# Kernel tuning notes

Measured on AMD Instinct MI355X. Metric: run time of the kernel, lower is better.

## Reference

```python
import jax, jax.numpy as jnp
import numpy as np

V, P, C, L, H = 50257, 1024, 768, 12, 12  # vocab, block_size, n_embd, n_layer, n_head
HD = C // H                                # head_dim = 64
B, T = 2, 1024
STD = 0.02
EPS = 1e-5


def setup_inputs() -> dict:
    key = jax.random.key(0)
    ks = jax.random.split(key, 8)
    n = lambda k, shape: (jax.random.normal(k, shape, dtype=jnp.float32) * STD)
    return dict(
        idx=jax.random.randint(ks[0], (B, T), 0, V),
        wte=n(ks[1], (V, C)),
        wpe=n(ks[2], (P, C)),
        ln1_g=jnp.ones((L, C), jnp.float32), ln1_b=jnp.zeros((L, C), jnp.float32),
        attn_w=n(ks[3], (L, C, 3 * C)), attn_b=jnp.zeros((L, 3 * C), jnp.float32),
        proj_w=n(ks[4], (L, C, C)), proj_b=jnp.zeros((L, C), jnp.float32),
        ln2_g=jnp.ones((L, C), jnp.float32), ln2_b=jnp.zeros((L, C), jnp.float32),
        fc_w=n(ks[5], (L, C, 4 * C)), fc_b=jnp.zeros((L, 4 * C), jnp.float32),
        fp_w=n(ks[6], (L, 4 * C, C)), fp_b=jnp.zeros((L, C), jnp.float32),
        lnf_g=jnp.ones((C,), jnp.float32), lnf_b=jnp.zeros((C,), jnp.float32),
    )


def _ln(x, g, b):
    m = jnp.mean(x, axis=-1, keepdims=True)
    v = jnp.var(x, axis=-1, keepdims=True)
    return (x - m) * jax.lax.rsqrt(v + EPS) * g + b


def _block(x, p):
    (g1, b1, aw, ab, pw, pb, g2, b2, fw, fb, fpw, fpb) = p
    Bd, Td, Cd = x.shape
    # attention
    h = _ln(x, g1, b1)
    qkv = h @ aw + ab                                  # [B,T,3C]
    qkv = qkv.reshape(Bd, Td, H, 3 * HD)               # faithful to reshape(B,T,H,3*hd)
    q, k, v = jnp.split(qkv, 3, axis=-1)               # each [B,T,H,hd]
    scale = jnp.asarray(1.0 / np.sqrt(HD), x.dtype)
    att = jnp.einsum('bthd,bshd->bhts', q, k) * scale  # [B,H,T,T]
    mask = jnp.tril(jnp.ones((Td, Td), x.dtype))
    att = att * mask - 1e9 * (1.0 - mask)
    att = jax.nn.softmax(att, axis=-1)
    o = jnp.einsum('bhts,bshd->bthd', att, v).reshape(Bd, Td, Cd)
    x = x + (o @ pw + pb)
    # MLP (exact gelu, as TF keras 'gelu' default)
    h2 = _ln(x, g2, b2)
    x = x + (jax.nn.gelu(h2 @ fw + fb, approximate=False) @ fpw + fpb)
    return x


def reference(idx, wte, wpe, ln1_g, ln1_b, attn_w, attn_b, proj_w, proj_b,
              ln2_g, ln2_b, fc_w, fc_b, fp_w, fp_b, lnf_g, lnf_b):
    Td = idx.shape[1]
    x = wte[idx] + wpe[:Td]                            # [B,T,C]
    layers = (ln1_g, ln1_b, attn_w, attn_b, proj_w, proj_b,
              ln2_g, ln2_b, fc_w, fc_b, fp_w, fp_b)

    def step(carry, p):
        return _block(carry, p), None

    x, _ = jax.lax.scan(step, x, layers)
    x = _ln(x, lnf_g, lnf_b)
    logits = x @ wte.T                                 # tied embedding head [B,T,V]
    return logits
```

## Files before the change

kernel.cpp:

```cpp
#include <hip/hip_runtime.h>
#include <cstdint>
#include <cstddef>

#define BT   2048
#define TT   1024
#define CC   768
#define HH   12
#define LL   12
#define VV   50257
#define VPAD 50304

typedef __attribute__((ext_vector_type(8))) short short8;
typedef __attribute__((ext_vector_type(4))) float float4v;

__device__ __forceinline__ short f2bf(float f) {
  union { float f; uint32_t u; } v; v.f = f;
  uint32_t r = v.u + 0x7FFFu + ((v.u >> 16) & 1u);
  return (short)(r >> 16);
}

__device__ __forceinline__ void gl2lds16(const short* g, const short* lds_base) {
  __builtin_amdgcn_global_load_lds(
      (const __attribute__((address_space(1))) void*)g,
      (__attribute__((address_space(3))) void*)lds_base, 16, 0, 0);
}

__global__ __launch_bounds__(256) void cast_pad_kernel(const float* __restrict__ in,
                                                       short* __restrict__ out,
                                                       long n_in, long n_out) {
  long i = ((long)blockIdx.x * 256 + threadIdx.x) * 4;
  if (i >= n_out) return;
#pragma unroll
  for (int j = 0; j < 4; ++j) {
    long k = i + j;
    if (k < n_out) out[k] = (k < n_in) ? f2bf(in[k]) : (short)0;
  }
}

__global__ __launch_bounds__(256) void transpose_cast_kernel(const float* __restrict__ in,
                                                             short* __restrict__ out,
                                                             int K, int N) {
  __shared__ float tile[32][33];
  int n0 = blockIdx.x * 32, k0 = blockIdx.y * 32;
  int c = threadIdx.x & 31, r = threadIdx.x >> 5;
#pragma unroll
  for (int rr = 0; rr < 32; rr += 8)
    tile[rr + r][c] = in[(size_t)(k0 + rr + r) * N + n0 + c];
  __syncthreads();
#pragma unroll
  for (int rr = 0; rr < 32; rr += 8)
    out[(size_t)(n0 + rr + r) * K + k0 + c] = f2bf(tile[c][rr + r]);
}

__global__ __launch_bounds__(256) void embed_kernel(const int* __restrict__ idx,
                                                    const float* __restrict__ wte,
                                                    const float* __restrict__ wpe,
                                                    float* __restrict__ x) {
  int row = blockIdx.x, tid = threadIdx.x;
  int tok = idx[row];
  int t = row & (TT - 1);
#pragma unroll
  for (int kk = 0; kk < 3; ++kk) {
    int c = tid + kk * 256;
    x[(size_t)row * CC + c] = wte[(size_t)tok * CC + c] + wpe[(size_t)t * CC + c];
  }
}

__global__ __launch_bounds__(256) void ln_kernel(const float* __restrict__ x,
                                                 const float* __restrict__ g,
                                                 const float* __restrict__ bta,
                                                 short* __restrict__ out) {
  int row = blockIdx.x, tid = threadIdx.x;
  const float* xr = x + (size_t)row * CC;
  float v0 = xr[tid], v1 = xr[tid + 256], v2 = xr[tid + 512];
  float s = v0 + v1 + v2;
#pragma unroll
  for (int off = 32; off >= 1; off >>= 1) s += __shfl_xor(s, off, 64);
  __shared__ float red[8];
  int wid = tid >> 6;
  if ((tid & 63) == 0) red[wid] = s;
  __syncthreads();
  float mean = (red[0] + red[1] + red[2] + red[3]) * (1.0f / CC);
  float d0 = v0 - mean, d1 = v1 - mean, d2 = v2 - mean;
  float q = d0 * d0 + d1 * d1 + d2 * d2;
#pragma unroll
  for (int off = 32; off >= 1; off >>= 1) q += __shfl_xor(q, off, 64);
  if ((tid & 63) == 0) red[4 + wid] = q;
  __syncthreads();
  float var = (red[4] + red[5] + red[6] + red[7]) * (1.0f / CC);
  float rstd = rsqrtf(var + 1e-5f);
  out[(size_t)row * CC + tid]       = f2bf(d0 * rstd * g[tid]       + bta[tid]);
  out[(size_t)row * CC + tid + 256] = f2bf(d1 * rstd * g[tid + 256] + bta[tid + 256]);
  out[(size_t)row * CC + tid + 512] = f2bf(d2 * rstd * g[tid + 512] + bta[tid + 512]);
}

template <int MODE>
__global__ __launch_bounds__(256) void gemm_nt(const short* __restrict__ A,
                                               const short* __restrict__ Bt,
                                               const float* __restrict__ bias,
                                               float* __restrict__ resf,
                                               short* __restrict__ outb,
                                               float* __restrict__ outf,
                                               int K, int ldo, int Nvalid) {
  __shared__ __align__(16) short As[128 * 32];
  __shared__ __align__(16) short Bs[128 * 32];
  const int tid = threadIdx.x;
  const int w = tid >> 6, lane = tid & 63, quad = lane >> 4, l16 = lane & 15;
  const int wr = w & 1, wc = w >> 1;
  const int m0 = blockIdx.y * 128, n0 = blockIdx.x * 128;

  float4v acc[4][4];
#pragma unroll
  for (int i = 0; i < 4; ++i)
#pragma unroll
    for (int j = 0; j < 4; ++j) acc[i][j] = float4v{0.f, 0.f, 0.f, 0.f};

  const int r0 = tid >> 2;
  const int c0 = (tid & 3) * 8;
  const short* ga0 = A  + (size_t)(m0 + r0) * K + c0;
  const short* ga1 = A  + (size_t)(m0 + 64 + r0) * K + c0;
  const short* gb0 = Bt + (size_t)(n0 + r0) * K + c0;
  const short* gb1 = Bt + (size_t)(n0 + 64 + r0) * K + c0;
  const short* lA0 = As + w * 512;
  const short* lA1 = As + 2048 + w * 512;
  const short* lB0 = Bs + w * 512;
  const short* lB1 = Bs + 2048 + w * 512;

  const int kTiles = K >> 5;
  for (int kt = 0; kt < kTiles; ++kt) {
    const int ko = kt * 32;
    __syncthreads();
    gl2lds16(ga0 + ko, lA0);
    gl2lds16(ga1 + ko, lA1);
    gl2lds16(gb0 + ko, lB0);
    gl2lds16(gb1 + ko, lB1);
    __syncthreads();
    short8 af[4], bfr[4];
#pragma unroll
    for (int t = 0; t < 4; ++t) {
      af[t]  = *(const short8*)&As[(wr * 64 + t * 16 + l16) * 32 + quad * 8];
      bfr[t] = *(const short8*)&Bs[(wc * 64 + t * 16 + l16) * 32 + quad * 8];
    }
#pragma unroll
    for (int i = 0; i < 4; ++i)
#pragma unroll
      for (int j = 0; j < 4; ++j)
        acc[i][j] = __builtin_amdgcn_mfma_f32_16x16x32_bf16(af[i], bfr[j], acc[i][j], 0, 0, 0);
  }

#pragma unroll
  for (int i = 0; i < 4; ++i) {
#pragma unroll
    for (int j = 0; j < 4; ++j) {
#pragma unroll
      for (int r = 0; r < 4; ++r) {
        int gm = m0 + wr * 64 + i * 16 + quad * 4 + r;
        int gn = n0 + wc * 64 + j * 16 + l16;
        float v = acc[i][j][r];
        if (MODE == 0) {
          outb[(size_t)gm * ldo + gn] = f2bf(v + bias[gn]);
        } else if (MODE == 1) {
          size_t o = (size_t)gm * ldo + gn;
          resf[o] = resf[o] + v + bias[gn];
        } else if (MODE == 2) {
          float t = v + bias[gn];
          float gl = 0.5f * t * (1.0f + erff(t * 0.70710678118654752f));
          outb[(size_t)gm * ldo + gn] = f2bf(gl);
        } else {
          if (gn < Nvalid) outf[(size_t)gm * ldo + gn] = v;
        }
      }
    }
  }
}

__global__ __launch_bounds__(256) void attn_kernel(const short* __restrict__ qkv,
                                                   short* __restrict__ o) {
  __shared__ __align__(16) short Vt[64 * 32];
  __shared__ __align__(16) short Pl[4][16 * 32];
  const int tid = threadIdx.x;
  const int w = tid >> 6, lane = tid & 63, quad = lane >> 4, l16 = lane & 15;
  const int b = blockIdx.z, h = blockIdx.y, q0 = blockIdx.x * 64;
  const size_t rs = 3 * CC;
  const size_t base = (size_t)b * TT * rs + (size_t)h * 192;

  short8 qa[2];
  {
    int t = q0 + w * 16 + l16;
    const short* qp = qkv + base + (size_t)t * rs + quad * 8;
    qa[0] = *(const short8*)(qp);
    qa[1] = *(const short8*)(qp + 32);
  }
  float4v oacc[4];
#pragma unroll
  for (int i = 0; i < 4; ++i) oacc[i] = float4v{0.f, 0.f, 0.f, 0.f};
  float mrun[4] = {-1e30f, -1e30f, -1e30f, -1e30f};
  float lrun[4] = {0.f, 0.f, 0.f, 0.f};

  const int nst = q0 / 32 + 2;
  for (int st = 0; st < nst; ++st) {
    const int s0 = st * 32;
    __syncthreads();
    {
      int sl = tid >> 3;
      int d0 = (tid & 7) * 8;
      const short* vp = qkv + base + (size_t)(s0 + sl) * rs + 128 + d0;
      short8 v8 = *(const short8*)vp;
#pragma unroll
      for (int j = 0; j < 8; ++j) Vt[(d0 + j) * 32 + sl] = v8[j];
    }
    __syncthreads();

    float4v S[2];
#pragma unroll
    for (int nt = 0; nt < 2; ++nt) {
      int s = s0 + nt * 16 + l16;
      const short* kp = qkv + base + (size_t)s * rs + 64 + quad * 8;
      short8 kb0 = *(const short8*)kp;
      short8 kb1 = *(const short8*)(kp + 32);
      float4v z = float4v{0.f, 0.f, 0.f, 0.f};
      z = __builtin_amdgcn_mfma_f32_16x16x32_bf16(qa[0], kb0, z, 0, 0, 0);
      z = __builtin_amdgcn_mfma_f32_16x16x32_bf16(qa[1], kb1, z, 0, 0, 0);
      S[nt] = z;
    }

#pragma unroll
    for (int r = 0; r < 4; ++r) {
      int trow = q0 + w * 16 + quad * 4 + r;
      float s0v = (s0 + l16      <= trow) ? S[0][r] * 0.125f : -1e30f;
      float s1v = (s0 + 16 + l16 <= trow) ? S[1][r] * 0.125f : -1e30f;
      float tm = fmaxf(s0v, s1v);
#pragma unroll
      for (int off = 1; off < 16; off <<= 1) tm = fmaxf(tm, __shfl_xor(tm, off, 64));
      float mnew = fmaxf(mrun[r], tm);
      float alpha = __expf(mrun[r] - mnew);
      mrun[r] = mnew;
      float p0 = __expf(s0v - mnew);
      float p1 = __expf(s1v - mnew);
      float rsum = p0 + p1;
#pragma unroll
      for (int off = 1; off < 16; off <<= 1) rsum += __shfl_xor(rsum, off, 64);
      lrun[r] = lrun[r] * alpha + rsum;
#pragma unroll
      for (int dc = 0; dc < 4; ++dc) oacc[dc][r] *= alpha;
      Pl[w][(quad * 4 + r) * 32 + l16]      = f2bf(p0);
      Pl[w][(quad * 4 + r) * 32 + 16 + l16] = f2bf(p1);
    }
    __syncthreads();

    short8 pa = *(const short8*)&Pl[w][l16 * 32 + quad * 8];
#pragma unroll
    for (int dc = 0; dc < 4; ++dc) {
      short8 vb = *(const short8*)&Vt[(dc * 16 + l16) * 32 + quad * 8];
      oacc[dc] = __builtin_amdgcn_mfma_f32_16x16x32_bf16(pa, vb, oacc[dc], 0, 0, 0);
    }
  }

#pragma unroll
  for (int dc = 0; dc < 4; ++dc)
#pragma unroll
    for (int r = 0; r < 4; ++r) {
      int t = q0 + w * 16 + quad * 4 + r;
      float val = oacc[dc][r] / lrun[r];
      o[(size_t)(b * TT + t) * CC + h * 64 + dc * 16 + l16] = f2bf(val);
    }
}

extern "C" void kernel_launch(void* const* d_in, const int* in_sizes, int n_in,
                              void* d_out, int out_size, void* d_ws, size_t ws_size,
                              hipStream_t stream) {
  const int*   idx   = (const int*)d_in[0];
  const float* wte   = (const float*)d_in[1];
  const float* wpe   = (const float*)d_in[2];
  const float* ln1g  = (const float*)d_in[3];
  const float* ln1b  = (const float*)d_in[4];
  const float* attnw = (const float*)d_in[5];
  const float* attnb = (const float*)d_in[6];
  const float* projw = (const float*)d_in[7];
  const float* projb = (const float*)d_in[8];
  const float* ln2g  = (const float*)d_in[9];
  const float* ln2b  = (const float*)d_in[10];
  const float* fcw   = (const float*)d_in[11];
  const float* fcb   = (const float*)d_in[12];
  const float* fpw   = (const float*)d_in[13];
  const float* fpb   = (const float*)d_in[14];
  const float* lnfg  = (const float*)d_in[15];
  const float* lnfb  = (const float*)d_in[16];
  float* out = (float*)d_out;

  char* p = (char*)d_ws;
  auto alloc = [&](size_t bytes) {
    char* r = p;
    p += (bytes + 255) & ~(size_t)255;
    return r;
  };
  short* wt_head = (short*)alloc((size_t)VPAD * CC * 2);
  short* wt_attn = (short*)alloc((size_t)3 * CC * CC * 2);
  short* wt_proj = (short*)alloc((size_t)CC * CC * 2);
  short* wt_fc   = (short*)alloc((size_t)4 * CC * CC * 2);
  short* wt_fp   = (short*)alloc((size_t)4 * CC * CC * 2);
  float* x       = (float*)alloc((size_t)BT * CC * 4);
  short* hbuf    = (short*)alloc((size_t)BT * CC * 2);
  short* obuf    = (short*)alloc((size_t)BT * CC * 2);
  short* qkvb    = (short*)alloc((size_t)BT * 3 * CC * 2);
  short* fcout   = (short*)alloc((size_t)BT * 4 * CC * 2);

  cast_pad_kernel<<<dim3(((long)VPAD * CC) / 1024), 256, 0, stream>>>(
      wte, wt_head, (long)VV * CC, (long)VPAD * CC);
  embed_kernel<<<dim3(BT), 256, 0, stream>>>(idx, wte, wpe, x);

  for (int l = 0; l < LL; ++l) {
    transpose_cast_kernel<<<dim3(2304 / 32, 768 / 32), 256, 0, stream>>>(
        attnw + (size_t)l * CC * 3 * CC, wt_attn, CC, 3 * CC);
    transpose_cast_kernel<<<dim3(768 / 32, 768 / 32), 256, 0, stream>>>(
        projw + (size_t)l * CC * CC, wt_proj, CC, CC);
    transpose_cast_kernel<<<dim3(3072 / 32, 768 / 32), 256, 0, stream>>>(
        fcw + (size_t)l * CC * 4 * CC, wt_fc, CC, 4 * CC);
    transpose_cast_kernel<<<dim3(768 / 32, 3072 / 32), 256, 0, stream>>>(
        fpw + (size_t)l * 4 * CC * CC, wt_fp, 4 * CC, CC);

    ln_kernel<<<dim3(BT), 256, 0, stream>>>(x, ln1g + l * CC, ln1b + l * CC, hbuf);
    gemm_nt<0><<<dim3(18, 16), 256, 0, stream>>>(
        hbuf, wt_attn, attnb + (size_t)l * 3 * CC, nullptr, qkvb, nullptr, CC, 3 * CC, 3 * CC);
    attn_kernel<<<dim3(TT / 64, HH, 2), 256, 0, stream>>>(qkvb, obuf);
    gemm_nt<1><<<dim3(6, 16), 256, 0, stream>>>(
        obuf, wt_proj, projb + (size_t)l * CC, x, nullptr, nullptr, CC, CC, CC);
    ln_kernel<<<dim3(BT), 256, 0, stream>>>(x, ln2g + l * CC, ln2b + l * CC, hbuf);
    gemm_nt<2><<<dim3(24, 16), 256, 0, stream>>>(
        hbuf, wt_fc, fcb + (size_t)l * 4 * CC, nullptr, fcout, nullptr, CC, 4 * CC, 4 * CC);
    gemm_nt<1><<<dim3(6, 16), 256, 0, stream>>>(
        fcout, wt_fp, fpb + (size_t)l * CC, x, nullptr, nullptr, 4 * CC, CC, CC);
  }

  ln_kernel<<<dim3(BT), 256, 0, stream>>>(x, lnfg, lnfb, hbuf);
  gemm_nt<3><<<dim3(VPAD / 128, 16), 256, 0, stream>>>(
      hbuf, wt_head, nullptr, nullptr, nullptr, out, CC, VV, VV);
}
```

Before: 4.143 ms.

## Batch weight transposes, add 64x64 GEMM for narrow outputs, swizzle head GEMM

When the workspace is large enough, all layers' weights are transposed and cast in four batched launches up front instead of 48 per-layer launches. The projection and MLP-down GEMMs (N=768) switch to a new 64x64-tile kernel, which gives 384 blocks instead of 96 and so fills more CUs. The logits GEMM uses a 1D grid with a block-index swizzle to improve L2 reuse, and writes its output with nontemporal stores. The embedding cast is vectorized with float4 loads and short4 stores. The smaller tiles reuse data less per block, and the batched path needs extra workspace.

```diff
diff --git a/kernel.cpp b/kernel.cpp
--- a/kernel.cpp
+++ b/kernel.cpp
@@ -11,6 +11,7 @@
 #define VPAD 50304
 
 typedef __attribute__((ext_vector_type(8))) short short8;
+typedef __attribute__((ext_vector_type(4))) short short4v;
 typedef __attribute__((ext_vector_type(4))) float float4v;
 
 __device__ __forceinline__ short f2bf(float f) {
@@ -30,16 +31,26 @@
                                                        long n_in, long n_out) {
   long i = ((long)blockIdx.x * 256 + threadIdx.x) * 4;
   if (i >= n_out) return;
-#pragma unroll
-  for (int j = 0; j < 4; ++j) {
-    long k = i + j;
-    if (k < n_out) out[k] = (k < n_in) ? f2bf(in[k]) : (short)0;
-  }
+  short4v o;
+  if (i + 4 <= n_in) {
+    float4v f = *(const float4v*)(in + i);
+    o[0] = f2bf(f[0]); o[1] = f2bf(f[1]); o[2] = f2bf(f[2]); o[3] = f2bf(f[3]);
+  } else {
+#pragma unroll
+    for (int j = 0; j < 4; ++j) {
+      long k = i + j;
+      o[j] = (k < n_in) ? f2bf(in[k]) : (short)0;
+    }
+  }
+  *(short4v*)(out + i) = o;
 }
 
 __global__ __launch_bounds__(256) void transpose_cast_kernel(const float* __restrict__ in,
                                                              short* __restrict__ out,
-                                                             int K, int N) {
+                                                             int K, int N,
+                                                             long ils, long ols) {
+  in  += (size_t)blockIdx.z * ils;
+  out += (size_t)blockIdx.z * ols;
   __shared__ float tile[32][33];
   int n0 = blockIdx.x * 32, k0 = blockIdx.y * 32;
   int c = threadIdx.x & 31, r = threadIdx.x >> 5;
@@ -94,7 +105,7 @@
   out[(size_t)row * CC + tid + 512] = f2bf(d2 * rstd * g[tid + 512] + bta[tid + 512]);
 }
 
-template <int MODE>
+template <int MODE, int SWZ = 0>
 __global__ __launch_bounds__(256) void gemm_nt(const short* __restrict__ A,
                                                const short* __restrict__ Bt,
                                                const float* __restrict__ bias,
@@ -107,7 +118,17 @@
   const int tid = threadIdx.x;
   const int w = tid >> 6, lane = tid & 63, quad = lane >> 4, l16 = lane & 15;
   const int wr = w & 1, wc = w >> 1;
-  const int m0 = blockIdx.y * 128, n0 = blockIdx.x * 128;
+
+  int bx, by;
+  if (SWZ) {
+    unsigned per = gridDim.x >> 3;
+    unsigned g = (blockIdx.x & 7u) * per + (blockIdx.x >> 3);
+    by = g & (BT / 128 - 1);
+    bx = g >> 4;
+  } else {
+    bx = blockIdx.x; by = blockIdx.y;
+  }
+  const int m0 = by * 128, n0 = bx * 128;
 
   float4v acc[4][4];
 #pragma unroll
@@ -167,7 +188,78 @@
           float gl = 0.5f * t * (1.0f + erff(t * 0.70710678118654752f));
           outb[(size_t)gm * ldo + gn] = f2bf(gl);
         } else {
-          if (gn < Nvalid) outf[(size_t)gm * ldo + gn] = v;
+          if (gn < Nvalid) __builtin_nontemporal_store(v, outf + (size_t)gm * ldo + gn);
+        }
+      }
+    }
+  }
+}
+
+template <int MODE>
+__global__ __launch_bounds__(256) void gemm_nt64(const short* __restrict__ A,
+                                                 const short* __restrict__ Bt,
+                                                 const float* __restrict__ bias,
+                                                 float* __restrict__ resf,
+                                                 short* __restrict__ outb,
+                                                 int K, int ldo) {
+  __shared__ __align__(16) short As[64 * 32];
+  __shared__ __align__(16) short Bs[64 * 32];
+  const int tid = threadIdx.x;
+  const int w = tid >> 6, lane = tid & 63, quad = lane >> 4, l16 = lane & 15;
+  const int wr = w & 1, wc = w >> 1;
+  const int m0 = blockIdx.y * 64, n0 = blockIdx.x * 64;
+
+  float4v acc[2][2];
+#pragma unroll
+  for (int i = 0; i < 2; ++i)
+#pragma unroll
+    for (int j = 0; j < 2; ++j) acc[i][j] = float4v{0.f, 0.f, 0.f, 0.f};
+
+  const int r0 = tid >> 2;
+  const int c0 = (tid & 3) * 8;
+  const short* ga = A  + (size_t)(m0 + r0) * K + c0;
+  const short* gb = Bt + (size_t)(n0 + r0) * K + c0;
+  const short* lA = As + w * 512;
+  const short* lB = Bs + w * 512;
+
+  const int kTiles = K >> 5;
+  for (int kt = 0; kt < kTiles; ++kt) {
+    const int ko = kt * 32;
+    __syncthreads();
+    gl2lds16(ga + ko, lA);
+    gl2lds16(gb + ko, lB);
+    __syncthreads();
+    short8 af[2], bfr[2];
+#pragma unroll
+    for (int t = 0; t < 2; ++t) {
+      af[t]  = *(const short8*)&As[(wr * 32 + t * 16 + l16) * 32 + quad * 8];
+      bfr[t] = *(const short8*)&Bs[(wc * 32 + t * 16 + l16) * 32 + quad * 8];
+    }
+#pragma unroll
+    for (int i = 0; i < 2; ++i)
+#pragma unroll
+      for (int j = 0; j < 2; ++j)
+        acc[i][j] = __builtin_amdgcn_mfma_f32_16x16x32_bf16(af[i], bfr[j], acc[i][j], 0, 0, 0);
+  }
+
+#pragma unroll
+  for (int i = 0; i < 2; ++i) {
+#pragma unroll
+    for (int j = 0; j < 2; ++j) {
+#pragma unroll
+      for (int r = 0; r < 4; ++r) {
+        int gm = m0 + wr * 32 + i * 16 + quad * 4 + r;
+        int gn = n0 + wc * 32 + j * 16 + l16;
+        float v = acc[i][j][r];
+        if (MODE == 0) {
+          outb[(size_t)gm * ldo + gn] = f2bf(v + bias[gn]);
+        } else if (MODE == 1) {
+          size_t o = (size_t)gm * ldo + gn;
+          resf[o] = resf[o] + v + bias[gn];
+        } else if (MODE == 2) {
+          float t = v + bias[gn];
+          float gl = 0.5f * t * (1.0f + erff(t * 0.70710678118654752f));
+          outb[(size_t)gm * ldo + gn] = f2bf(gl);
         }
       }
     }
@@ -294,11 +386,19 @@
     p += (bytes + 255) & ~(size_t)255;
     return r;
   };
+
+  const size_t SZ_ATTN = (size_t)3 * CC * CC * 2;
+  const size_t SZ_PROJ = (size_t)CC * CC * 2;
+  const size_t SZ_FC   = (size_t)4 * CC * CC * 2;
+  const size_t SZ_FP   = (size_t)4 * CC * CC * 2;
+  const bool big = ws_size >= (size_t)300 * 1024 * 1024;
+  const int wmul = big ? LL : 1;
+
   short* wt_head = (short*)alloc((size_t)VPAD * CC * 2);
-  short* wt_attn = (short*)alloc((size_t)3 * CC * CC * 2);
-  short* wt_proj = (short*)alloc((size_t)CC * CC * 2);
-  short* wt_fc   = (short*)alloc((size_t)4 * CC * CC * 2);
-  short* wt_fp   = (short*)alloc((size_t)4 * CC * CC * 2);
+  short* wt_attn = (short*)alloc(SZ_ATTN * wmul);
+  short* wt_proj = (short*)alloc(SZ_PROJ * wmul);
+  short* wt_fc   = (short*)alloc(SZ_FC * wmul);
+  short* wt_fp   = (short*)alloc(SZ_FP * wmul);
   float* x       = (float*)alloc((size_t)BT * CC * 4);
   short* hbuf    = (short*)alloc((size_t)BT * CC * 2);
   short* obuf    = (short*)alloc((size_t)BT * CC * 2);
@@ -309,30 +409,48 @@
       wte, wt_head, (long)VV * CC, (long)VPAD * CC);
   embed_kernel<<<dim3(BT), 256, 0, stream>>>(idx, wte, wpe, x);
 
+  if (big) {
+    transpose_cast_kernel<<<dim3(2304 / 32, 768 / 32, LL), 256, 0, stream>>>(
+        attnw, wt_attn, CC, 3 * CC, (long)CC * 3 * CC, (long)3 * CC * CC);
+    transpose_cast_kernel<<<dim3(768 / 32, 768 / 32, LL), 256, 0, stream>>>(
+        projw, wt_proj, CC, CC, (long)CC * CC, (long)CC * CC);
+    transpose_cast_kernel<<<dim3(3072 / 32, 768 / 32, LL), 256, 0, stream>>>(
+        fcw, wt_fc, CC, 4 * CC, (long)CC * 4 * CC, (long)4 * CC * CC);
+    transpose_cast_kernel<<<dim3(768 / 32, 3072 / 32, LL), 256, 0, stream>>>(
+        fpw, wt_fp, 4 * CC, CC, (long)4 * CC * CC, (long)4 * CC * CC);
+  }
+
   for (int l = 0; l < LL; ++l) {
-    transpose_cast_kernel<<<dim3(2304 / 32, 768 / 32), 256, 0, stream>>>(
-        attnw + (size_t)l * CC * 3 * CC, wt_attn, CC, 3 * CC);
-    transpose_cast_kernel<<<dim3(768 / 32, 768 / 32), 256, 0, stream>>>(
-        projw + (size_t)l * CC * CC, wt_proj, CC, CC);
-    transpose_cast_kernel<<<dim3(3072 / 32, 768 / 32), 256, 0, stream>>>(
-        fcw + (size_t)l * CC * 4 * CC, wt_fc, CC, 4 * CC);
-    transpose_cast_kernel<<<dim3(768 / 32, 3072 / 32), 256, 0, stream>>>(
-        fpw + (size_t)l * 4 * CC * CC, wt_fp, 4 * CC, CC);
+    const short* wa = wt_attn + (big ? (size_t)l * 3 * CC * CC : 0);
+    const short* wp = wt_proj + (big ? (size_t)l * CC * CC : 0);
+    const short* wf = wt_fc   + (big ? (size_t)l * 4 * CC * CC : 0);
+    const short* wq = wt_fp   + (big ? (size_t)l * 4 * CC * CC : 0);
+
+    if (!big) {
+      transpose_cast_kernel<<<dim3(2304 / 32, 768 / 32, 1), 256, 0, stream>>>(
+          attnw + (size_t)l * CC * 3 * CC, wt_attn, CC, 3 * CC, 0, 0);
+      transpose_cast_kernel<<<dim3(768 / 32, 768 / 32, 1), 256, 0, stream>>>(
+          projw + (size_t)l * CC * CC, wt_proj, CC, CC, 0, 0);
+      transpose_cast_kernel<<<dim3(3072 / 32, 768 / 32, 1), 256, 0, stream>>>(
+          fcw + (size_t)l * CC * 4 * CC, wt_fc, CC, 4 * CC, 0, 0);
+      transpose_cast_kernel<<<dim3(768 / 32, 3072 / 32, 1), 256, 0, stream>>>(
+          fpw + (size_t)l * 4 * CC * CC, wt_fp, 4 * CC, CC, 0, 0);
+    }
 
     ln_kernel<<<dim3(BT), 256, 0, stream>>>(x, ln1g + l * CC, ln1b + l * CC, hbuf);
     gemm_nt<0><<<dim3(18, 16), 256, 0, stream>>>(
-        hbuf, wt_attn, attnb + (size_t)l * 3 * CC, nullptr, qkvb, nullptr, CC, 3 * CC, 3 * CC);
+        hbuf, wa, attnb + (size_t)l * 3 * CC, nullptr, qkvb, nullptr, CC, 3 * CC, 3 * CC);
     attn_kernel<<<dim3(TT / 64, HH, 2), 256, 0, stream>>>(qkvb, obuf);
-    gemm_nt<1><<<dim3(6, 16), 256, 0, stream>>>(
-        obuf, wt_proj, projb + (size_t)l * CC, x, nullptr, nullptr, CC, CC, CC);
+    gemm_nt64<1><<<dim3(12, 32), 256, 0, stream>>>(
+        obuf, wp, projb + (size_t)l * CC, x, nullptr, CC, CC);
     ln_kernel<<<dim3(BT), 256, 0, stream>>>(x, ln2g + l * CC, ln2b + l * CC, hbuf);
     gemm_nt<2><<<dim3(24, 16), 256, 0, stream>>>(
-        hbuf, wt_fc, fcb + (size_t)l * 4 * CC, nullptr, fcout, nullptr, CC, 4 * CC, 4 * CC);
-    gemm_nt<1><<<dim3(6, 16), 256, 0, stream>>>(
-        fcout, wt_fp, fpb + (size_t)l * CC, x, nullptr, nullptr, 4 * CC, CC, CC);
+        hbuf, wf, fcb + (size_t)l * 4 * CC, nullptr, fcout, nullptr, CC, 4 * CC, 4 * CC);
+    gemm_nt64<1><<<dim3(12, 32), 256, 0, stream>>>(
+        fcout, wq, fpb + (size_t)l * CC, x, nullptr, 4 * CC, CC);
   }
 
   ln_kernel<<<dim3(BT), 256, 0, stream>>>(x, lnfg, lnfb, hbuf);
-  gemm_nt<3><<<dim3(VPAD / 128, 16), 256, 0, stream>>>(
+  gemm_nt<3, 1><<<dim3((VPAD / 128) * 16), 256, 0, stream>>>(
       hbuf, wt_head, nullptr, nullptr, nullptr, out, CC, VV, VV);
 }
```

New measurement: 3.607 ms. 12.9% less time.
